# Kernel optimization log

Measured on AMD Instinct MI355X. Metric: run time of the kernel, lower is better.

## Reference

```python
import jax, jax.numpy as jnp
import numpy as np

B, C, D, H, W = 2, 256, 16, 64, 64


def _conv1x1(x, w, b):
    # 1x1x1 Conv3d == pointwise channel matmul. x: [B,C,D,H,W], w: [Cout,Cin], b: [Cout]
    return jnp.einsum('bcdhw,oc->bodhw', x, w) + b[None, :, None, None, None]


def setup_inputs() -> dict:
    key = jax.random.key(0)
    ks = jax.random.split(key, 12)
    wscale = 1.0 / np.sqrt(C)  # keep pre-softmax logits in a sane range
    inp = {
        'eeg_input': jax.random.normal(ks[0], (B, C, D, H, W), jnp.float32),
        'image_input': jax.random.normal(ks[1], (B, C, D, H, W), jnp.float32),
        'q_w': jax.random.normal(ks[2], (C, C), jnp.float32) * wscale,
        'q_b': jnp.zeros((C,), jnp.float32),
        'k_w': jax.random.normal(ks[3], (C, C), jnp.float32) * wscale,
        'k_b': jnp.zeros((C,), jnp.float32),
        'v_w': jax.random.normal(ks[4], (C, C), jnp.float32) * wscale,
        'v_b': jnp.zeros((C,), jnp.float32),
        'attn_w': jax.random.normal(ks[5], (C, C), jnp.float32) * wscale,
        'attn_b': jnp.zeros((C,), jnp.float32),
        'out_w': jax.random.normal(ks[6], (C, C), jnp.float32) * wscale,
        'out_b': jnp.zeros((C,), jnp.float32),
    }
    return inp


def reference(eeg_input, image_input, q_w, q_b, k_w, k_b, v_w, v_b,
              attn_w, attn_b, out_w, out_b):
    q = _conv1x1(eeg_input, q_w, q_b)      # [B,C,D,H,W]
    k = _conv1x1(image_input, k_w, k_b)    # [B,C,D,H,W]
    v = _conv1x1(image_input, v_w, v_b)    # [B,C,D,H,W]
    # torch.matmul(q, k.transpose(-2,-1)): contract over W -> scores [B,C,D,H,H]
    scores = jax.nn.softmax(jnp.einsum('bcdhw,bcdxw->bcdhx', q, k), axis=-1)
    wv = jnp.einsum('bcdhx,bcdxw->bcdhw', scores, v)  # [B,C,D,H,W]
    a = jax.nn.relu(_conv1x1(wv, attn_w, attn_b))
    return jax.nn.relu(_conv1x1(a, out_w, out_b))
```

## Files before the change

### kernel.cpp

```cpp
#include <hip/hip_runtime.h>

#define CC   256
#define DHWC 65536
#define NBC  2

typedef __attribute__((ext_vector_type(8))) short bf16x8;
typedef __attribute__((ext_vector_type(4))) short bf16x4;
typedef __attribute__((ext_vector_type(4))) float f32x4;

__device__ __forceinline__ short f2bf(float x) {
    unsigned u = __builtin_bit_cast(unsigned, x);
    unsigned r = (u + 0x7fffu + ((u >> 16) & 1u)) >> 16;
    return (short)r;
}
__device__ __forceinline__ float bf2f(short h) {
    unsigned u = ((unsigned)(unsigned short)h) << 16;
    return __builtin_bit_cast(float, u);
}

__device__ __forceinline__ int swz(int r, int c) {
    return (r * 128 + c * 2) ^ ((r & 7) << 4);
}
__device__ __forceinline__ int vswz(int r, int c) {
    return (r * 128 + c * 2) ^ (((r ^ (r >> 3)) & 7) << 4);
}
__device__ __forceinline__ int swz512(int s, int k) {
    return (s * 512 + k * 2) ^ ((s & 7) << 4);
}
__device__ __forceinline__ int swz256(int r, int s) {
    return (r * 256 + s * 2) ^ ((r & 7) << 4);
}

__global__ void prep_w_kernel(const float* __restrict__ q_w, const float* __restrict__ k_w,
                              const float* __restrict__ v_w, const float* __restrict__ attn_w,
                              const float* __restrict__ out_w, short* __restrict__ wsp)
{
    const int l  = threadIdx.x;
    const int fo = blockIdx.x;
    const int t  = blockIdx.y;
    const int m  = blockIdx.z;
    const float* w = (m == 0) ? q_w : (m == 1) ? k_w : (m == 2) ? v_w
                   : (m == 3) ? attn_w : out_w;
    short* whi = wsp + (size_t)m * 131072;
    short* wlo = whi + 65536;

    const int o = fo * 16 + (l & 15);
    const int k = t * 32 + (l >> 4) * 8;

    bf16x8 hv, lv;
    #pragma unroll
    for (int r = 0; r < 8; ++r) {
        const float x = w[o * 256 + k + r];
        const short h = f2bf(x);
        hv[r] = h;
        lv[r] = f2bf(x - bf2f(h));
    }
    const int idx = (fo * 8 + t) * 64 + l;
    *(bf16x8*)(whi + idx * 8) = hv;
    *(bf16x8*)(wlo + idx * 8) = lv;
}

__global__ __launch_bounds__(1024, 4) void conv_mfma_kernel(
    const float* __restrict__ x, const short* __restrict__ whi,
    const short* __restrict__ wlo, const float* __restrict__ bias,
    float* __restrict__ out)
{
    __shared__ char lds[65536];

    const int tid  = threadIdx.x;
    const int lane = tid & 63;
    const int wave = tid >> 6;
    const size_t boff = (size_t)blockIdx.y * ((size_t)CC * DHWC);
    const int sT = blockIdx.x * 128;
    const float* xb = x + boff + sT;
    const bf16x8* whf = (const bf16x8*)whi;
    const bf16x8* wlf = (const bf16x8*)wlo;

    f32x4 acc[8];
    #pragma unroll
    for (int j = 0; j < 8; ++j) acc[j] = (f32x4){0.f, 0.f, 0.f, 0.f};

    const int s_l = tid & 127;
    const int k8  = tid >> 7;

    float xr[8];
    #pragma unroll
    for (int r = 0; r < 8; ++r)
        xr[r] = xb[(size_t)(k8 * 8 + r) * DHWC + s_l];
    {
        bf16x8 hv, lv;
        #pragma unroll
        for (int r = 0; r < 8; ++r) {
            const short h = f2bf(xr[r]);
            hv[r] = h;
            lv[r] = f2bf(xr[r] - bf2f(h));
        }
        const int off = swz(s_l, k8 * 8);
        *(bf16x8*)(lds + off) = hv;
        *(bf16x8*)(lds + 16384 + off) = lv;
    }

    #pragma unroll
    for (int t = 0; t < 4; ++t) {
        if (t < 3) {
            #pragma unroll
            for (int r = 0; r < 8; ++r)
                xr[r] = xb[(size_t)((t + 1) * 64 + k8 * 8 + r) * DHWC + s_l];
        }
        __syncthreads();

        const char* bhib = lds + (t & 1) * 32768;
        const char* blob = bhib + 16384;
        #pragma unroll
        for (int kk = 0; kk < 2; ++kk) {
            const int idx = (wave * 8 + 2 * t + kk) * 64 + lane;
            const bf16x8 a1h = whf[idx];
            const bf16x8 a1l = wlf[idx];
            #pragma unroll
            for (int j = 0; j < 8; ++j) {
                const int s = j * 16 + (lane & 15);
                const int k = kk * 32 + (lane >> 4) * 8;
                const bf16x8 bh = *(const bf16x8*)(bhib + swz(s, k));
                const bf16x8 bl = *(const bf16x8*)(blob + swz(s, k));
                f32x4 c = acc[j];
                c = __builtin_amdgcn_mfma_f32_16x16x32_bf16(a1h, bh, c, 0, 0, 0);
                c = __builtin_amdgcn_mfma_f32_16x16x32_bf16(a1h, bl, c, 0, 0, 0);
                c = __builtin_amdgcn_mfma_f32_16x16x32_bf16(a1l, bh, c, 0, 0, 0);
                acc[j] = c;
            }
        }

        if (t < 3) {
            bf16x8 hv, lv;
            #pragma unroll
            for (int r = 0; r < 8; ++r) {
                const short h = f2bf(xr[r]);
                hv[r] = h;
                lv[r] = f2bf(xr[r] - bf2f(h));
            }
            const int off = ((t + 1) & 1) * 32768 + swz(s_l, k8 * 8);
            *(bf16x8*)(lds + off) = hv;
            *(bf16x8*)(lds + 16384 + off) = lv;
        }
    }

    float* ob = out + boff + sT;
    const int n_l = lane & 15;
    const int m4  = (lane >> 4) * 4;
    #pragma unroll
    for (int r = 0; r < 4; ++r) {
        const int o = wave * 16 + m4 + r;
        const float bv = bias[o];
        #pragma unroll
        for (int j = 0; j < 8; ++j)
            ob[(size_t)o * DHWC + j * 16 + n_l] = acc[j][r] + bv;
    }
}

__global__ __launch_bounds__(1024, 4) void kv_conv_kernel(
    const float* __restrict__ img,
    const short* __restrict__ wkhi, const short* __restrict__ wklo,
    const short* __restrict__ wvhi, const short* __restrict__ wvlo,
    const float* __restrict__ kb, const float* __restrict__ vb,
    float* __restrict__ kout, short* __restrict__ vout)
{
    __shared__ char lds[65536];

    const int tid  = threadIdx.x;
    const int lane = tid & 63;
    const int wave = tid >> 6;
    const size_t boff = (size_t)blockIdx.y * ((size_t)CC * DHWC);
    const int sT = blockIdx.x * 128;
    const float* xb = img + boff + sT;
    const bf16x8* wkhf = (const bf16x8*)wkhi;
    const bf16x8* wklf = (const bf16x8*)wklo;
    const bf16x8* wvhf = (const bf16x8*)wvhi;
    const bf16x8* wvlf = (const bf16x8*)wvlo;

    f32x4 acck[8], accv[8];
    #pragma unroll
    for (int j = 0; j < 8; ++j) {
        acck[j] = (f32x4){0.f, 0.f, 0.f, 0.f};
        accv[j] = (f32x4){0.f, 0.f, 0.f, 0.f};
    }

    const int s_l = tid & 127;
    const int k8  = tid >> 7;

    float xr[8];
    #pragma unroll
    for (int r = 0; r < 8; ++r)
        xr[r] = xb[(size_t)(k8 * 8 + r) * DHWC + s_l];
    {
        bf16x8 hv, lv;
        #pragma unroll
        for (int r = 0; r < 8; ++r) {
            const short h = f2bf(xr[r]);
            hv[r] = h;
            lv[r] = f2bf(xr[r] - bf2f(h));
        }
        const int off = swz(s_l, k8 * 8);
        *(bf16x8*)(lds + off) = hv;
        *(bf16x8*)(lds + 16384 + off) = lv;
    }

    #pragma unroll
    for (int t = 0; t < 4; ++t) {
        if (t < 3) {
            #pragma unroll
            for (int r = 0; r < 8; ++r)
                xr[r] = xb[(size_t)((t + 1) * 64 + k8 * 8 + r) * DHWC + s_l];
        }
        __syncthreads();

        const char* bhib = lds + (t & 1) * 32768;
        const char* blob = bhib + 16384;
        #pragma unroll
        for (int kk = 0; kk < 2; ++kk) {
            const int idx = (wave * 8 + 2 * t + kk) * 64 + lane;
            const bf16x8 akh = wkhf[idx];
            const bf16x8 akl = wklf[idx];
            const bf16x8 avh = wvhf[idx];
            const bf16x8 avl = wvlf[idx];
            #pragma unroll
            for (int j = 0; j < 8; ++j) {
                const int s = j * 16 + (lane & 15);
                const int k = kk * 32 + (lane >> 4) * 8;
                const bf16x8 bh = *(const bf16x8*)(bhib + swz(s, k));
                const bf16x8 bl = *(const bf16x8*)(blob + swz(s, k));
                f32x4 c = acck[j];
                c = __builtin_amdgcn_mfma_f32_16x16x32_bf16(akh, bh, c, 0, 0, 0);
                c = __builtin_amdgcn_mfma_f32_16x16x32_bf16(akh, bl, c, 0, 0, 0);
                c = __builtin_amdgcn_mfma_f32_16x16x32_bf16(akl, bh, c, 0, 0, 0);
                acck[j] = c;
                f32x4 d = accv[j];
                d = __builtin_amdgcn_mfma_f32_16x16x32_bf16(avh, bh, d, 0, 0, 0);
                d = __builtin_amdgcn_mfma_f32_16x16x32_bf16(avh, bl, d, 0, 0, 0);
                d = __builtin_amdgcn_mfma_f32_16x16x32_bf16(avl, bh, d, 0, 0, 0);
                accv[j] = d;
            }
        }

        if (t < 3) {
            bf16x8 hv, lv;
            #pragma unroll
            for (int r = 0; r < 8; ++r) {
                const short h = f2bf(xr[r]);
                hv[r] = h;
                lv[r] = f2bf(xr[r] - bf2f(h));
            }
            const int off = ((t + 1) & 1) * 32768 + swz(s_l, k8 * 8);
            *(bf16x8*)(lds + off) = hv;
            *(bf16x8*)(lds + 16384 + off) = lv;
        }
    }

    float* ko = kout + boff + sT;
    const int n_l = lane & 15;
    const int m4  = (lane >> 4) * 4;
    #pragma unroll
    for (int r = 0; r < 4; ++r) {
        const int o = wave * 16 + m4 + r;
        const float kbv = kb[o];
        #pragma unroll
        for (int j = 0; j < 8; ++j)
            ko[(size_t)o * DHWC + j * 16 + n_l] = acck[j][r] + kbv;
    }

    __syncthreads();
    #pragma unroll
    for (int r = 0; r < 4; ++r) {
        const int o = wave * 16 + m4 + r;
        const float vbv = vb[o];
        #pragma unroll
        for (int j = 0; j < 8; ++j)
            *(short*)(lds + swz256(o, j * 16 + n_l)) = f2bf(accv[j][r] + vbv);
    }
    __syncthreads();
    short* vo = vout + boff + sT;
    #pragma unroll
    for (int it = 0; it < 4; ++it) {
        const int row = it * 64 + wave * 4 + (lane >> 4);
        const int sc  = (lane & 15) * 8;
        const bf16x8 v8 = *(const bf16x8*)(lds + swz256(row, sc));
        *(bf16x8*)(vo + (size_t)row * DHWC + sc) = v8;
    }
}

template<int WVM>
__global__ __launch_bounds__(256, 4) void attn_mfma_kernel(
    const float* q, const float* __restrict__ kg,
    const short* __restrict__ vsh, float* wvf, short* __restrict__ wvs)
{
    __shared__ char lds[40960];
    const int QHI = 0, QLO = 8192, KHI = 16384, KLO = 24576, VT = 32768;

    const int tid  = threadIdx.x;
    const int lane = tid & 63;
    const int wsx  = tid >> 6;
    const size_t base = (size_t)blockIdx.x * 4096;

    {
        const int r  = tid >> 2;
        const int cb = (tid & 3) * 16;
        #pragma unroll
        for (int half = 0; half < 2; ++half) {
            const int c = cb + half * 8;
            const float4 qa = *(const float4*)(q  + base + r * 64 + c);
            const float4 qb = *(const float4*)(q  + base + r * 64 + c + 4);
            const float4 ka = *(const float4*)(kg + base + r * 64 + c);
            const float4 kb = *(const float4*)(kg + base + r * 64 + c + 4);
            bf16x8 qh, ql, kh, kl;
            #pragma unroll
            for (int e = 0; e < 4; ++e) {
                float xq = ((const float*)&qa)[e];
                short h = f2bf(xq); qh[e] = h; ql[e] = f2bf(xq - bf2f(h));
                xq = ((const float*)&qb)[e];
                h = f2bf(xq); qh[e + 4] = h; ql[e + 4] = f2bf(xq - bf2f(h));
                float xk = ((const float*)&ka)[e];
                h = f2bf(xk); kh[e] = h; kl[e] = f2bf(xk - bf2f(h));
                xk = ((const float*)&kb)[e];
                h = f2bf(xk); kh[e + 4] = h; kl[e + 4] = f2bf(xk - bf2f(h));
            }
            const int off = swz(r, c);
            *(bf16x8*)(lds + QHI + off) = qh;
            *(bf16x8*)(lds + QLO + off) = ql;
            *(bf16x8*)(lds + KHI + off) = kh;
            *(bf16x8*)(lds + KLO + off) = kl;
        }
        const short* vpl = vsh + base;
        const int x0 = (tid >> 4) * 4;
        const int w0 = (tid & 15) * 4;
        bf16x4 vr[4];
        #pragma unroll
        for (int i = 0; i < 4; ++i)
            vr[i] = *(const bf16x4*)(vpl + (x0 + i) * 64 + w0);
        #pragma unroll
        for (int j = 0; j < 4; ++j) {
            bf16x4 tv;
            #pragma unroll
            for (int i = 0; i < 4; ++i) tv[i] = vr[i][j];
            *(bf16x4*)(lds + VT + vswz(w0 + j, x0)) = tv;
        }
    }
    __syncthreads();

    f32x4 acc[4];
    #pragma unroll
    for (int j = 0; j < 4; ++j) acc[j] = (f32x4){0.f, 0.f, 0.f, 0.f};

    const int arow = wsx * 16 + (lane & 15);
    #pragma unroll
    for (int kk = 0; kk < 2; ++kk) {
        const int kcol = kk * 32 + (lane >> 4) * 8;
        const bf16x8 aqh = *(const bf16x8*)(lds + QHI + swz(arow, kcol));
        const bf16x8 aql = *(const bf16x8*)(lds + QLO + swz(arow, kcol));
        #pragma unroll
        for (int j = 0; j < 4; ++j) {
            const int brow = j * 16 + (lane & 15);
            const bf16x8 bkh = *(const bf16x8*)(lds + KHI + swz(brow, kcol));
            const bf16x8 bkl = *(const bf16x8*)(lds + KLO + swz(brow, kcol));
            f32x4 c = acc[j];
            c = __builtin_amdgcn_mfma_f32_16x16x32_bf16(aqh, bkh, c, 0, 0, 0);
            c = __builtin_amdgcn_mfma_f32_16x16x32_bf16(aqh, bkl, c, 0, 0, 0);
            c = __builtin_amdgcn_mfma_f32_16x16x32_bf16(aql, bkh, c, 0, 0, 0);
            acc[j] = c;
        }
    }

    float p[4][4], invs[4];
    #pragma unroll
    for (int r = 0; r < 4; ++r) {
        float m = fmaxf(fmaxf(acc[0][r], acc[1][r]), fmaxf(acc[2][r], acc[3][r]));
        m = fmaxf(m, __shfl_xor(m, 1));
        m = fmaxf(m, __shfl_xor(m, 2));
        m = fmaxf(m, __shfl_xor(m, 4));
        m = fmaxf(m, __shfl_xor(m, 8));
        float s = 0.f;
        #pragma unroll
        for (int j = 0; j < 4; ++j) { p[j][r] = __expf(acc[j][r] - m); s += p[j][r]; }
        s += __shfl_xor(s, 1);
        s += __shfl_xor(s, 2);
        s += __shfl_xor(s, 4);
        s += __shfl_xor(s, 8);
        invs[r] = 1.f / s;
    }

    __syncthreads();

    #pragma unroll
    for (int r = 0; r < 4; ++r) {
        const int row = wsx * 16 + (lane >> 4) * 4 + r;
        #pragma unroll
        for (int j = 0; j < 4; ++j) {
            const int col = j * 16 + (lane & 15);
            *(short*)(lds + QHI + swz(row, col)) = f2bf(p[j][r]);
        }
    }
    __syncthreads();

    f32x4 o_[4];
    #pragma unroll
    for (int j = 0; j < 4; ++j) o_[j] = (f32x4){0.f, 0.f, 0.f, 0.f};

    #pragma unroll
    for (int kk = 0; kk < 2; ++kk) {
        const int kcol = kk * 32 + (lane >> 4) * 8;
        const bf16x8 aph = *(const bf16x8*)(lds + QHI + swz(arow, kcol));
        #pragma unroll
        for (int j = 0; j < 4; ++j) {
            const int brow = j * 16 + (lane & 15);
            const bf16x8 bvh = *(const bf16x8*)(lds + VT + vswz(brow, kcol));
            o_[j] = __builtin_amdgcn_mfma_f32_16x16x32_bf16(aph, bvh, o_[j], 0, 0, 0);
        }
    }

    if (WVM == 0) {
        #pragma unroll
        for (int r = 0; r < 4; ++r) {
            const int h = wsx * 16 + (lane >> 4) * 4 + r;
            #pragma unroll
            for (int j = 0; j < 4; ++j)
                wvf[base + (size_t)h * 64 + j * 16 + (lane & 15)] = o_[j][r] * invs[r];
        }
    } else {
        __syncthreads();
        #pragma unroll
        for (int r = 0; r < 4; ++r) {
            const int h = wsx * 16 + (lane >> 4) * 4 + r;
            #pragma unroll
            for (int j = 0; j < 4; ++j)
                *(short*)(lds + QHI + swz(h, j * 16 + (lane & 15))) = f2bf(o_[j][r] * invs[r]);
        }
        __syncthreads();
        #pragma unroll
        for (int it = 0; it < 4; ++it) {
            const int row = it * 16 + (tid >> 4);
            const int sc  = (tid & 15) * 4;
            bf16x4 v4;
            v4 = *(const bf16x4*)(lds + QHI + ((row * 128 + sc * 2) ^ ((row & 7) << 4)));
            *(bf16x4*)(wvs + base + (size_t)row * 64 + sc) = v4;
        }
    }
}

template<int IM>
__global__ __launch_bounds__(1024, 4) void tail_fused_kernel(
    const float* __restrict__ xf, const short* __restrict__ xs,
    const short* __restrict__ w1hi, const short* __restrict__ w1lo,
    const float* __restrict__ b1,
    const short* __restrict__ w2hi, const short* __restrict__ w2lo,
    const float* __restrict__ b2,
    float* __restrict__ out)
{
    __shared__ char lds[65536];

    const int tid  = threadIdx.x;
    const int lane = tid & 63;
    const int wave = tid >> 6;
    const size_t boff = (size_t)blockIdx.y * ((size_t)CC * DHWC);
    const int sT = blockIdx.x * 128;
    const bf16x8* w1hf = (const bf16x8*)w1hi;
    const bf16x8* w1lf = (const bf16x8*)w1lo;

    f32x4 acc[8];
    #pragma unroll
    for (int j = 0; j < 8; ++j) acc[j] = (f32x4){0.f, 0.f, 0.f, 0.f};

    const int s_l = tid & 127;
    const int k8  = tid >> 7;
    const float* xbf = xf + boff + sT;
    const short* xbs = xs + boff + sT;

    float xr[8];
    short sr[8];
    if (IM == 0) {
        #pragma unroll
        for (int r = 0; r < 8; ++r)
            xr[r] = xbf[(size_t)(k8 * 8 + r) * DHWC + s_l];
        bf16x8 hv, lv;
        #pragma unroll
        for (int r = 0; r < 8; ++r) {
            const short h = f2bf(xr[r]);
            hv[r] = h;
            lv[r] = f2bf(xr[r] - bf2f(h));
        }
        const int off = swz(s_l, k8 * 8);
        *(bf16x8*)(lds + off) = hv;
        *(bf16x8*)(lds + 16384 + off) = lv;
    } else {
        #pragma unroll
        for (int r = 0; r < 8; ++r)
            sr[r] = xbs[(size_t)(k8 * 8 + r) * DHWC + s_l];
        bf16x8 hv;
        #pragma unroll
        for (int r = 0; r < 8; ++r) hv[r] = sr[r];
        *(bf16x8*)(lds + swz(s_l, k8 * 8)) = hv;
    }

    #pragma unroll
    for (int t = 0; t < 4; ++t) {
        if (t < 3) {
            if (IM == 0) {
                #pragma unroll
                for (int r = 0; r < 8; ++r)
                    xr[r] = xbf[(size_t)((t + 1) * 64 + k8 * 8 + r) * DHWC + s_l];
            } else {
                #pragma unroll
                for (int r = 0; r < 8; ++r)
                    sr[r] = xbs[(size_t)((t + 1) * 64 + k8 * 8 + r) * DHWC + s_l];
            }
        }
        __syncthreads();

        const char* bhib = lds + (t & 1) * (IM == 0 ? 32768 : 16384);
        const char* blob = bhib + 16384;
        #pragma unroll
        for (int kk = 0; kk < 2; ++kk) {
            const int idx = (wave * 8 + 2 * t + kk) * 64 + lane;
            const bf16x8 a1h = w1hf[idx];
            const bf16x8 a1l = w1lf[idx];
            #pragma unroll
            for (int j = 0; j < 8; ++j) {
                const int s = j * 16 + (lane & 15);
                const int k = kk * 32 + (lane >> 4) * 8;
                const bf16x8 bh = *(const bf16x8*)(bhib + swz(s, k));
                f32x4 c = acc[j];
                c = __builtin_amdgcn_mfma_f32_16x16x32_bf16(a1h, bh, c, 0, 0, 0);
                c = __builtin_amdgcn_mfma_f32_16x16x32_bf16(a1l, bh, c, 0, 0, 0);
                if (IM == 0) {
                    const bf16x8 bl = *(const bf16x8*)(blob + swz(s, k));
                    c = __builtin_amdgcn_mfma_f32_16x16x32_bf16(a1h, bl, c, 0, 0, 0);
                }
                acc[j] = c;
            }
        }

        if (t < 3) {
            const int off = ((t + 1) & 1) * (IM == 0 ? 32768 : 16384) + swz(s_l, k8 * 8);
            if (IM == 0) {
                bf16x8 hv, lv;
                #pragma unroll
                for (int r = 0; r < 8; ++r) {
                    const short h = f2bf(xr[r]);
                    hv[r] = h;
                    lv[r] = f2bf(xr[r] - bf2f(h));
                }
                *(bf16x8*)(lds + off) = hv;
                *(bf16x8*)(lds + 16384 + off) = lv;
            } else {
                bf16x8 hv;
                #pragma unroll
                for (int r = 0; r < 8; ++r) hv[r] = sr[r];
                *(bf16x8*)(lds + off) = hv;
            }
        }
    }

    __syncthreads();
    {
        const int m4 = (lane >> 4) * 4;
        #pragma unroll
        for (int r = 0; r < 4; ++r) {
            const int o = wave * 16 + m4 + r;
            const float bv = b1[o];
            #pragma unroll
            for (int j = 0; j < 8; ++j) {
                const int s = j * 16 + (lane & 15);
                *(short*)(lds + swz512(s, o)) = f2bf(fmaxf(acc[j][r] + bv, 0.f));
            }
        }
    }
    __syncthreads();

    f32x4 acc2[8];
    #pragma unroll
    for (int j = 0; j < 8; ++j) acc2[j] = (f32x4){0.f, 0.f, 0.f, 0.f};

    const bf16x8* w2hf = (const bf16x8*)w2hi;
    const bf16x8* w2lf = (const bf16x8*)w2lo;
    #pragma unroll
    for (int t2 = 0; t2 < 8; ++t2) {
        const int idx = (wave * 8 + t2) * 64 + lane;
        const bf16x8 a2h = w2hf[idx];
        const bf16x8 a2l = w2lf[idx];
        #pragma unroll
        for (int j = 0; j < 8; ++j) {
            const int s = j * 16 + (lane & 15);
            const int k = t2 * 32 + (lane >> 4) * 8;
            const bf16x8 bh = *(const bf16x8*)(lds + swz512(s, k));
            f32x4 c = acc2[j];
            c = __builtin_amdgcn_mfma_f32_16x16x32_bf16(a2h, bh, c, 0, 0, 0);
            c = __builtin_amdgcn_mfma_f32_16x16x32_bf16(a2l, bh, c, 0, 0, 0);
            acc2[j] = c;
        }
    }

    float* ob = out + boff + sT;
    const int n_l = lane & 15;
    const int m4  = (lane >> 4) * 4;
    #pragma unroll
    for (int r = 0; r < 4; ++r) {
        const int o = wave * 16 + m4 + r;
        const float bv = b2[o];
        #pragma unroll
        for (int j = 0; j < 8; ++j)
            ob[(size_t)o * DHWC + j * 16 + n_l] = fmaxf(acc2[j][r] + bv, 0.f);
    }
}

extern "C" void kernel_launch(void* const* d_in, const int* in_sizes, int n_in,
                              void* d_out, int out_size, void* d_ws, size_t ws_size,
                              hipStream_t stream)
{
    const float* eeg    = (const float*)d_in[0];
    const float* img    = (const float*)d_in[1];
    const float* q_w    = (const float*)d_in[2];
    const float* q_b    = (const float*)d_in[3];
    const float* k_w    = (const float*)d_in[4];
    const float* k_b    = (const float*)d_in[5];
    const float* v_w    = (const float*)d_in[6];
    const float* v_b    = (const float*)d_in[7];
    const float* attn_w = (const float*)d_in[8];
    const float* attn_b = (const float*)d_in[9];
    const float* out_w  = (const float*)d_in[10];
    const float* out_b  = (const float*)d_in[11];

    const size_t N = (size_t)NBC * CC * DHWC;
    float* qbuf = (float*)d_ws;
    float* kbuf = qbuf + N;
    const size_t need_rich = 4 * N + 4 * N + 2 * N + (size_t)5 * 131072 * 2;
    const bool rich = (ws_size >= need_rich);
    short* wvs = rich ? (short*)(kbuf + N) : (short*)nullptr;
    short* wsp = rich ? (wvs + N) : (short*)(kbuf + N);
    short* vsh  = (short*)d_out;
    float* outp = (float*)d_out;

    prep_w_kernel<<<dim3(16, 8, 5), dim3(64), 0, stream>>>(
        q_w, k_w, v_w, attn_w, out_w, wsp);

    const dim3 cgrid(DHWC / 128, NBC);

    conv_mfma_kernel<<<cgrid, dim3(1024), 0, stream>>>(
        eeg, wsp, wsp + 65536, q_b, qbuf);

    kv_conv_kernel<<<cgrid, dim3(1024), 0, stream>>>(
        img, wsp + 131072, wsp + 131072 + 65536,
        wsp + 2 * 131072, wsp + 2 * 131072 + 65536,
        k_b, v_b, kbuf, vsh);

    if (rich) {
        attn_mfma_kernel<1><<<dim3(NBC * CC * 16), dim3(256), 0, stream>>>(
            qbuf, kbuf, vsh, (float*)nullptr, wvs);
        tail_fused_kernel<1><<<cgrid, dim3(1024), 0, stream>>>(
            (const float*)nullptr, wvs,
            wsp + 3 * 131072, wsp + 3 * 131072 + 65536, attn_b,
            wsp + 4 * 131072, wsp + 4 * 131072 + 65536, out_b, outp);
    } else {
        attn_mfma_kernel<0><<<dim3(NBC * CC * 16), dim3(256), 0, stream>>>(
            qbuf, kbuf, vsh, qbuf, (short*)nullptr);
        tail_fused_kernel<0><<<cgrid, dim3(1024), 0, stream>>>(
            qbuf, (const short*)nullptr,
            wsp + 3 * 131072, wsp + 3 * 131072 + 65536, attn_b,
            wsp + 4 * 131072, wsp + 4 * 131072 + 65536, out_b, outp);
    }
}
```

Before: 392.6 us.

## Stage K output through LDS and write bf16 attention output in place over K

The K projection output is now staged through swizzled LDS in two halves, so global stores become coalesced float4 row writes instead of strided scalar stores. The attention kernel always produces bf16 output, writing each block's slab in place over its own K region of the buffer with a doubled stride. The tail kernel reads that interleaved layout. This removes the float32 fallback path and the separate workspace buffer. Attention loads are restructured to use float4-sized chunks. It depends on each block reading its K tile into LDS before overwriting that same memory, and it adds extra barriers in the K conv epilogue.

```diff
diff --git a/kernel.cpp b/kernel.cpp
--- a/kernel.cpp
+++ b/kernel.cpp
@@ -29,6 +29,9 @@
 }
 __device__ __forceinline__ int swz256(int r, int s) {
     return (r * 256 + s * 2) ^ ((r & 7) << 4);
+}
+__device__ __forceinline__ int swzf(int r, int c) {
+    return (r * 512 + c * 4) ^ ((r & 7) << 4);
 }
 
 __global__ void prep_w_kernel(const float* __restrict__ q_w, const float* __restrict__ k_w,
@@ -255,16 +258,32 @@
         }
     }
 
-    float* ko = kout + boff + sT;
     const int n_l = lane & 15;
     const int m4  = (lane >> 4) * 4;
-    #pragma unroll
-    for (int r = 0; r < 4; ++r) {
-        const int o = wave * 16 + m4 + r;
-        const float kbv = kb[o];
-        #pragma unroll
-        for (int j = 0; j < 8; ++j)
-            ko[(size_t)o * DHWC + j * 16 + n_l] = acck[j][r] + kbv;
+
+    float* ko = kout + boff + sT;
+    #pragma unroll
+    for (int h = 0; h < 2; ++h) {
+        __syncthreads();
+        if ((wave >> 3) == h) {
+            #pragma unroll
+            for (int r = 0; r < 4; ++r) {
+                const int o = wave * 16 + m4 + r;
+                const float kbv = kb[o];
+                const int lr = o & 127;
+                #pragma unroll
+                for (int j = 0; j < 8; ++j)
+                    *(float*)(lds + swzf(lr, j * 16 + n_l)) = acck[j][r] + kbv;
+            }
+        }
+        __syncthreads();
+        #pragma unroll
+        for (int it = 0; it < 4; ++it) {
+            const int lr = it * 32 + (tid >> 5);
+            const int c4 = (tid & 31) * 4;
+            const float4 vv = *(const float4*)(lds + swzf(lr, c4));
+            *(float4*)(ko + (size_t)(h * 128 + lr) * DHWC + c4) = vv;
+        }
     }
 
     __syncthreads();
@@ -287,10 +306,9 @@
     }
 }
 
-template<int WVM>
 __global__ __launch_bounds__(256, 4) void attn_mfma_kernel(
-    const float* q, const float* __restrict__ kg,
-    const short* __restrict__ vsh, float* wvf, short* __restrict__ wvs)
+    const float* __restrict__ q, const float* kg,
+    const short* __restrict__ vsh, short* wvk)
 {
     __shared__ char lds[40960];
     const int QHI = 0, QLO = 8192, KHI = 16384, KLO = 24576, VT = 32768;
@@ -301,32 +319,25 @@
     const size_t base = (size_t)blockIdx.x * 4096;
 
     {
-        const int r  = tid >> 2;
-        const int cb = (tid & 3) * 16;
-        #pragma unroll
-        for (int half = 0; half < 2; ++half) {
-            const int c = cb + half * 8;
+        #pragma unroll
+        for (int it = 0; it < 4; ++it) {
+            const int r = it * 16 + (tid >> 4);
+            const int c = (tid & 15) * 4;
             const float4 qa = *(const float4*)(q  + base + r * 64 + c);
-            const float4 qb = *(const float4*)(q  + base + r * 64 + c + 4);
             const float4 ka = *(const float4*)(kg + base + r * 64 + c);
-            const float4 kb = *(const float4*)(kg + base + r * 64 + c + 4);
-            bf16x8 qh, ql, kh, kl;
+            bf16x4 qh, ql, kh, kl;
             #pragma unroll
             for (int e = 0; e < 4; ++e) {
-                float xq = ((const float*)&qa)[e];
+                const float xq = ((const float*)&qa)[e];
                 short h = f2bf(xq); qh[e] = h; ql[e] = f2bf(xq - bf2f(h));
-                xq = ((const float*)&qb)[e];
-                h = f2bf(xq); qh[e + 4] = h; ql[e + 4] = f2bf(xq - bf2f(h));
-                float xk = ((const float*)&ka)[e];
+                const float xk = ((const float*)&ka)[e];
                 h = f2bf(xk); kh[e] = h; kl[e] = f2bf(xk - bf2f(h));
-                xk = ((const float*)&kb)[e];
-                h = f2bf(xk); kh[e + 4] = h; kl[e + 4] = f2bf(xk - bf2f(h));
             }
             const int off = swz(r, c);
-            *(bf16x8*)(lds + QHI + off) = qh;
-            *(bf16x8*)(lds + QLO + off) = ql;
-            *(bf16x8*)(lds + KHI + off) = kh;
-            *(bf16x8*)(lds + KLO + off) = kl;
+            *(bf16x4*)(lds + QHI + off) = qh;
+            *(bf16x4*)(lds + QLO + off) = ql;
+            *(bf16x4*)(lds + KHI + off) = kh;
+            *(bf16x4*)(lds + KLO + off) = kl;
         }
         const short* vpl = vsh + base;
         const int x0 = (tid >> 4) * 4;
@@ -415,38 +426,27 @@
         }
     }
 
-    if (WVM == 0) {
-        #pragma unroll
-        for (int r = 0; r < 4; ++r) {
-            const int h = wsx * 16 + (lane >> 4) * 4 + r;
-            #pragma unroll
-            for (int j = 0; j < 4; ++j)
-                wvf[base + (size_t)h * 64 + j * 16 + (lane & 15)] = o_[j][r] * invs[r];
-        }
-    } else {
-        __syncthreads();
-        #pragma unroll
-        for (int r = 0; r < 4; ++r) {
-            const int h = wsx * 16 + (lane >> 4) * 4 + r;
-            #pragma unroll
-            for (int j = 0; j < 4; ++j)
-                *(short*)(lds + QHI + swz(h, j * 16 + (lane & 15))) = f2bf(o_[j][r] * invs[r]);
-        }
-        __syncthreads();
-        #pragma unroll
-        for (int it = 0; it < 4; ++it) {
-            const int row = it * 16 + (tid >> 4);
-            const int sc  = (tid & 15) * 4;
-            bf16x4 v4;
-            v4 = *(const bf16x4*)(lds + QHI + ((row * 128 + sc * 2) ^ ((row & 7) << 4)));
-            *(bf16x4*)(wvs + base + (size_t)row * 64 + sc) = v4;
-        }
-    }
-}
-
-template<int IM>
+    __syncthreads();
+    #pragma unroll
+    for (int r = 0; r < 4; ++r) {
+        const int h = wsx * 16 + (lane >> 4) * 4 + r;
+        #pragma unroll
+        for (int j = 0; j < 4; ++j)
+            *(short*)(lds + QHI + swz(h, j * 16 + (lane & 15))) = f2bf(o_[j][r] * invs[r]);
+    }
+    __syncthreads();
+    short* wvo = wvk + (size_t)blockIdx.x * 8192;
+    #pragma unroll
+    for (int it = 0; it < 4; ++it) {
+        const int row = it * 16 + (tid >> 4);
+        const int sc  = (tid & 15) * 4;
+        const bf16x4 v4 = *(const bf16x4*)(lds + QHI + swz(row, sc));
+        *(bf16x4*)(wvo + (size_t)row * 64 + sc) = v4;
+    }
+}
+
 __global__ __launch_bounds__(1024, 4) void tail_fused_kernel(
-    const float* __restrict__ xf, const short* __restrict__ xs,
+    const short* __restrict__ xs,
     const short* __restrict__ w1hi, const short* __restrict__ w1lo,
     const float* __restrict__ b1,
     const short* __restrict__ w2hi, const short* __restrict__ w2lo,
@@ -469,29 +469,15 @@
 
     const int s_l = tid & 127;
     const int k8  = tid >> 7;
-    const float* xbf = xf + boff + sT;
-    const short* xbs = xs + boff + sT;
-
-    float xr[8];
+
+    const short* xslab = xs + (size_t)blockIdx.y * 33554432
+                            + (size_t)(sT >> 12) * 8192 + (sT & 4095);
+
     short sr[8];
-    if (IM == 0) {
-        #pragma unroll
-        for (int r = 0; r < 8; ++r)
-            xr[r] = xbf[(size_t)(k8 * 8 + r) * DHWC + s_l];
-        bf16x8 hv, lv;
-        #pragma unroll
-        for (int r = 0; r < 8; ++r) {
-            const short h = f2bf(xr[r]);
-            hv[r] = h;
-            lv[r] = f2bf(xr[r] - bf2f(h));
-        }
-        const int off = swz(s_l, k8 * 8);
-        *(bf16x8*)(lds + off) = hv;
-        *(bf16x8*)(lds + 16384 + off) = lv;
-    } else {
-        #pragma unroll
-        for (int r = 0; r < 8; ++r)
-            sr[r] = xbs[(size_t)(k8 * 8 + r) * DHWC + s_l];
+    #pragma unroll
+    for (int r = 0; r < 8; ++r)
+        sr[r] = xslab[(size_t)(k8 * 8 + r) * 131072 + s_l];
+    {
         bf16x8 hv;
         #pragma unroll
         for (int r = 0; r < 8; ++r) hv[r] = sr[r];
@@ -501,20 +487,13 @@
     #pragma unroll
     for (int t = 0; t < 4; ++t) {
         if (t < 3) {
-            if (IM == 0) {
-                #pragma unroll
-                for (int r = 0; r < 8; ++r)
-                    xr[r] = xbf[(size_t)((t + 1) * 64 + k8 * 8 + r) * DHWC + s_l];
-            } else {
-                #pragma unroll
-                for (int r = 0; r < 8; ++r)
-                    sr[r] = xbs[(size_t)((t + 1) * 64 + k8 * 8 + r) * DHWC + s_l];
-            }
+            #pragma unroll
+            for (int r = 0; r < 8; ++r)
+                sr[r] = xslab[(size_t)((t + 1) * 64 + k8 * 8 + r) * 131072 + s_l];
         }
         __syncthreads();
 
-        const char* bhib = lds + (t & 1) * (IM == 0 ? 32768 : 16384);
-        const char* blob = bhib + 16384;
+        const char* bhib = lds + (t & 1) * 16384;
         #pragma unroll
         for (int kk = 0; kk < 2; ++kk) {
             const int idx = (wave * 8 + 2 * t + kk) * 64 + lane;
@@ -528,32 +507,15 @@
                 f32x4 c = acc[j];
                 c = __builtin_amdgcn_mfma_f32_16x16x32_bf16(a1h, bh, c, 0, 0, 0);
                 c = __builtin_amdgcn_mfma_f32_16x16x32_bf16(a1l, bh, c, 0, 0, 0);
-                if (IM == 0) {
-                    const bf16x8 bl = *(const bf16x8*)(blob + swz(s, k));
-                    c = __builtin_amdgcn_mfma_f32_16x16x32_bf16(a1h, bl, c, 0, 0, 0);
-                }
                 acc[j] = c;
             }
         }
 
         if (t < 3) {
-            const int off = ((t + 1) & 1) * (IM == 0 ? 32768 : 16384) + swz(s_l, k8 * 8);
-            if (IM == 0) {
-                bf16x8 hv, lv;
-                #pragma unroll
-                for (int r = 0; r < 8; ++r) {
-                    const short h = f2bf(xr[r]);
-                    hv[r] = h;
-                    lv[r] = f2bf(xr[r] - bf2f(h));
-                }
-                *(bf16x8*)(lds + off) = hv;
-                *(bf16x8*)(lds + 16384 + off) = lv;
-            } else {
-                bf16x8 hv;
-                #pragma unroll
-                for (int r = 0; r < 8; ++r) hv[r] = sr[r];
-                *(bf16x8*)(lds + off) = hv;
-            }
+            bf16x8 hv;
+            #pragma unroll
+            for (int r = 0; r < 8; ++r) hv[r] = sr[r];
+            *(bf16x8*)(lds + ((t + 1) & 1) * 16384 + swz(s_l, k8 * 8)) = hv;
         }
     }
 
@@ -629,10 +591,7 @@
     const size_t N = (size_t)NBC * CC * DHWC;
     float* qbuf = (float*)d_ws;
     float* kbuf = qbuf + N;
-    const size_t need_rich = 4 * N + 4 * N + 2 * N + (size_t)5 * 131072 * 2;
-    const bool rich = (ws_size >= need_rich);
-    short* wvs = rich ? (short*)(kbuf + N) : (short*)nullptr;
-    short* wsp = rich ? (wvs + N) : (short*)(kbuf + N);
+    short* wsp  = (short*)(kbuf + N);
     short* vsh  = (short*)d_out;
     float* outp = (float*)d_out;
 
@@ -649,19 +608,11 @@
         wsp + 2 * 131072, wsp + 2 * 131072 + 65536,
         k_b, v_b, kbuf, vsh);
 
-    if (rich) {
-        attn_mfma_kernel<1><<<dim3(NBC * CC * 16), dim3(256), 0, stream>>>(
-            qbuf, kbuf, vsh, (float*)nullptr, wvs);
-        tail_fused_kernel<1><<<cgrid, dim3(1024), 0, stream>>>(
-            (const float*)nullptr, wvs,
-            wsp + 3 * 131072, wsp + 3 * 131072 + 65536, attn_b,
-            wsp + 4 * 131072, wsp + 4 * 131072 + 65536, out_b, outp);
-    } else {
-        attn_mfma_kernel<0><<<dim3(NBC * CC * 16), dim3(256), 0, stream>>>(
-            qbuf, kbuf, vsh, qbuf, (short*)nullptr);
-        tail_fused_kernel<0><<<cgrid, dim3(1024), 0, stream>>>(
-            qbuf, (const short*)nullptr,
-            wsp + 3 * 131072, wsp + 3 * 131072 + 65536, attn_b,
-            wsp + 4 * 131072, wsp + 4 * 131072 + 65536, out_b, outp);
-    }
-}
+    attn_mfma_kernel<<<dim3(NBC * CC * 16), dim3(256), 0, stream>>>(
+        qbuf, kbuf, vsh, (short*)kbuf);
+
+    tail_fused_kernel<<<cgrid, dim3(1024), 0, stream>>>(
+        (const short*)kbuf,
+        wsp + 3 * 131072, wsp + 3 * 131072 + 65536, attn_b,
+        wsp + 4 * 131072, wsp + 4 * 131072 + 65536, out_b, outp);
+}
```

After: 374.3 us. 4.7% less time.
